# Performance work log

Hardware: AMD Instinct MI355X
Metric: run time of the kernel (lower is better)

Reference implementation:

```python
import jax, jax.numpy as jnp
import numpy as np

N = 50000
E = 800000
IN_C = 128
OUT_C = 256
NUM_REL = 6


def _rgcn_conv(x, src, dst, etype, W, root, bias):
    # PyG RGCNConv (no bases, aggr='mean'):
    # out = x @ root + bias + sum_r mean_{j in N_r(i)}(x_j) @ W[r]
    n = x.shape[0]
    xe = x[src]  # [E, d_in] gather of source features
    out = x @ root + bias
    for r in range(NUM_REL):
        m = (etype == r)
        s = jax.ops.segment_sum(jnp.where(m[:, None], xe, 0.0), dst, num_segments=n)
        c = jax.ops.segment_sum(m.astype(x.dtype), dst, num_segments=n)
        out = out + (s / jnp.maximum(c, 1.0)[:, None]) @ W[r]
    return out


def setup_inputs() -> dict:
    key = jax.random.key(0)
    ks = jax.random.split(key, 16)
    half = OUT_C // 2

    def g(k, shape, fan_in):
        return jax.random.normal(k, shape, dtype=jnp.float32) / np.sqrt(fan_in)

    return {
        "x": jax.random.normal(ks[0], (N, IN_C), dtype=jnp.float32),
        "edge_index": jax.random.randint(ks[1], (2, E), 0, N, dtype=jnp.int32),
        "edge_type": jax.random.randint(ks[2], (E,), 0, NUM_REL, dtype=jnp.int32),
        # encoder MLP
        "enc_w0": g(ks[3], (IN_C, OUT_C), IN_C), "enc_b0": jnp.zeros((OUT_C,), jnp.float32),
        "enc_w1": g(ks[4], (OUT_C, OUT_C), OUT_C), "enc_b1": jnp.zeros((OUT_C,), jnp.float32),
        "enc_w2": g(ks[5], (OUT_C, half), OUT_C), "enc_b2": jnp.zeros((half,), jnp.float32),
        # conv1
        "W1": g(ks[6], (NUM_REL, IN_C, OUT_C), IN_C), "root1": g(ks[7], (IN_C, OUT_C), IN_C),
        "b1": jnp.zeros((OUT_C,), jnp.float32),
        # conv2
        "W2": g(ks[8], (NUM_REL, OUT_C, OUT_C), OUT_C), "root2": g(ks[9], (OUT_C, OUT_C), OUT_C),
        "b2": jnp.zeros((OUT_C,), jnp.float32),
        # conv_out
        "W3": g(ks[10], (NUM_REL, OUT_C, half), OUT_C), "root3": g(ks[11], (OUT_C, half), OUT_C),
        "b3": jnp.zeros((half,), jnp.float32),
    }


def reference(x, edge_index, edge_type,
              enc_w0, enc_b0, enc_w1, enc_b1, enc_w2, enc_b2,
              W1, root1, b1, W2, root2, b2, W3, root3, b3):
    src, dst = edge_index[0], edge_index[1]
    # dense encoder branch
    h = jax.nn.relu(x @ enc_w0 + enc_b0)
    h = jax.nn.relu(h @ enc_w1 + enc_b1)
    self_feat = h @ enc_w2 + enc_b2
    # RGCN branch
    g1 = jax.nn.relu(_rgcn_conv(x, src, dst, edge_type, W1, root1, b1))
    g2 = jax.nn.relu(_rgcn_conv(g1, src, dst, edge_type, W2, root2, b2))
    graph_feat = _rgcn_conv(g2, src, dst, edge_type, W3, root3, b3)
    return jnp.concatenate([self_feat, graph_feat], axis=-1)
```

## Files before the change

kernel.cpp:

```cpp
#include <hip/hip_runtime.h>

#define NN   50000
#define EE   800000
#define INC  128
#define OUTC 256
#define HALF 128
#define NREL 6
#define NCELL (NN * NREL)

typedef __attribute__((ext_vector_type(4))) short s16x4;
typedef __attribute__((ext_vector_type(8))) short bf16x8;
typedef __attribute__((ext_vector_type(4))) float f32x4;

__device__ __forceinline__ float b2f(short b) {
    unsigned u = ((unsigned)(unsigned short)b) << 16;
    return __uint_as_float(u);
}
__device__ __forceinline__ short f2b(float f) {
    unsigned u = __float_as_uint(f);
    unsigned r = (u + 0x7fffu + ((u >> 16) & 1u)) >> 16;
    return (short)r;
}

__device__ __forceinline__ void gload16(const void* g, void* l) {
    __builtin_amdgcn_global_load_lds(
        (const __attribute__((address_space(1))) void*)g,
        (__attribute__((address_space(3))) void*)l, 16, 0, 0);
}

__global__ __launch_bounds__(256) void count_k(const int* __restrict__ dst,
                                               const int* __restrict__ et,
                                               int* __restrict__ cnt) {
    int e = blockIdx.x * 256 + threadIdx.x;
    if (e < EE) atomicAdd(&cnt[dst[e] * NREL + et[e]], 1);
}

__global__ __launch_bounds__(256) void scanA_k(const int* __restrict__ cnt,
                                               int* __restrict__ off,
                                               int* __restrict__ bsum, int n) {
    __shared__ int sh[256];
    int t = threadIdx.x;
    int base = blockIdx.x * 512 + t * 2;
    int v0 = (base < n) ? cnt[base] : 0;
    int v1 = (base + 1 < n) ? cnt[base + 1] : 0;
    int s = v0 + v1;
    sh[t] = s; __syncthreads();
    for (int o = 1; o < 256; o <<= 1) {
        int u = (t >= o) ? sh[t - o] : 0;
        __syncthreads();
        sh[t] += u;
        __syncthreads();
    }
    int excl = sh[t] - s;
    if (base < n)     off[base]     = excl;
    if (base + 1 < n) off[base + 1] = excl + v0;
    if (t == 255) bsum[blockIdx.x] = sh[255];
}

__global__ __launch_bounds__(1024) void scanB_k(int* __restrict__ bsum, int nb) {
    __shared__ int sh[1024];
    int t = threadIdx.x;
    int s = (t < nb) ? bsum[t] : 0;
    sh[t] = s; __syncthreads();
    for (int o = 1; o < 1024; o <<= 1) {
        int u = (t >= o) ? sh[t - o] : 0;
        __syncthreads();
        sh[t] += u;
        __syncthreads();
    }
    if (t < nb) bsum[t] = sh[t] - s;
}

__global__ __launch_bounds__(256) void scanC_k(int* __restrict__ off,
                                               const int* __restrict__ bsum, int n) {
    int i = blockIdx.x * 256 + threadIdx.x;
    if (i < n) off[i] += bsum[i >> 9];
    if (i == 0) off[n] = EE;
}

__global__ __launch_bounds__(256) void copyint_k(const int* __restrict__ a,
                                                 int* __restrict__ b, int n) {
    int i = blockIdx.x * 256 + threadIdx.x;
    if (i < n) b[i] = a[i];
}

__global__ __launch_bounds__(256) void fill_k(const int* __restrict__ src,
                                              const int* __restrict__ dst,
                                              const int* __restrict__ et,
                                              int* __restrict__ cur,
                                              int* __restrict__ es) {
    int e = blockIdx.x * 256 + threadIdx.x;
    if (e < EE) {
        int key = dst[e] * NREL + et[e];
        int p = atomicAdd(&cur[key], 1);
        es[p] = src[e];
    }
}

__global__ __launch_bounds__(256) void cast_x_k(const float* __restrict__ x,
                                                short* __restrict__ xb, int n4) {
    int i = blockIdx.x * 256 + threadIdx.x;
    if (i < n4) {
        float4 v = ((const float4*)x)[i];
        s16x4 o;
        o[0] = f2b(v.x); o[1] = f2b(v.y); o[2] = f2b(v.z); o[3] = f2b(v.w);
        ((s16x4*)xb)[i] = o;
    }
}

__global__ __launch_bounds__(256) void wtcat_k(const float* __restrict__ root,
                                               const float* __restrict__ W,
                                               int K0, int Ktot, int Ncols,
                                               short* __restrict__ WT) {
    int i = blockIdx.x * 256 + threadIdx.x;
    if (i >= Ncols * Ktot) return;
    int n = i / Ktot, k = i - n * Ktot;
    float v = (k < K0) ? root[(size_t)k * Ncols + n]
                       : W[(size_t)(k - K0) * Ncols + n];
    WT[(size_t)n * Ktot + k] = f2b(v);
}

template<int D>
__global__ __launch_bounds__(256) void agg_k(const short* __restrict__ X, int ldx,
                                             const int* __restrict__ off,
                                             const int* __restrict__ es,
                                             short* __restrict__ AG, int lda,
                                             int node0, int ncells) {
    constexpr int LPC = D / 4;
    int sub  = threadIdx.x / LPC;
    int lane = threadIdx.x % LPC;
    int ci = blockIdx.x * (256 / LPC) + sub;
    if (ci >= ncells) return;
    int node = ci / NREL, rel = ci - node * NREL;
    int gcell = (node0 + node) * NREL + rel;
    int beg = off[gcell], end = off[gcell + 1];
    int c0 = lane * 4;
    float s0 = 0.f, s1 = 0.f, s2 = 0.f, s3 = 0.f;
    int j = beg;
    for (; j + 1 < end; j += 2) {
        s16x4 v = *(const s16x4*)(X + (size_t)es[j] * ldx + c0);
        s16x4 w = *(const s16x4*)(X + (size_t)es[j + 1] * ldx + c0);
        s0 += b2f(v[0]) + b2f(w[0]);
        s1 += b2f(v[1]) + b2f(w[1]);
        s2 += b2f(v[2]) + b2f(w[2]);
        s3 += b2f(v[3]) + b2f(w[3]);
    }
    if (j < end) {
        s16x4 v = *(const s16x4*)(X + (size_t)es[j] * ldx + c0);
        s0 += b2f(v[0]); s1 += b2f(v[1]); s2 += b2f(v[2]); s3 += b2f(v[3]);
    }
    float inv = (end > beg) ? 1.f / (float)(end - beg) : 0.f;
    s16x4 o;
    o[0] = f2b(s0 * inv); o[1] = f2b(s1 * inv);
    o[2] = f2b(s2 * inv); o[3] = f2b(s3 * inv);
    *(s16x4*)(AG + (size_t)node * lda + rel * D + c0) = o;
}

#define ACH(R, q) ((((R) << 2) | ((q) ^ ((R) & 3) ^ (((R) >> 2) & 1))) * 8)

__global__ __launch_bounds__(256) void gemm_bt_k(
    const short* __restrict__ A0, int ld0,
    const short* __restrict__ A1, int ld1, int Ksplit,
    const short* __restrict__ BT,
    int M, int K, int Ncols,
    const float* __restrict__ bias, int relu,
    short* __restrict__ Cb, int ldcb,
    float* __restrict__ Cf, int ldcf) {
    __shared__ __align__(16) short As[2][128 * 32];
    __shared__ __align__(16) short Bs[2][128 * 32];
    const int tid = threadIdx.x;
    const int wave = tid >> 6, lane = tid & 63;
    const int wm = (wave & 1) * 64, wn = (wave >> 1) * 64;
    const int l16 = lane & 15, quad = lane >> 4;
    const int bm = blockIdx.x * 128, bn = blockIdx.y * 128;

    const int s0 = tid, s1 = tid + 256;
    const int r0 = s0 >> 2, c0 = (s0 & 3) ^ (r0 & 3) ^ ((r0 >> 2) & 1);
    const int r1 = s1 >> 2, c1 = (s1 & 3) ^ (r1 & 3) ^ ((r1 >> 2) & 1);

    auto stage = [&](int buf, int k0) {
        const short* Ab; int lda; int kk;
        if (k0 < Ksplit) { Ab = A0; lda = ld0; kk = k0; }
        else             { Ab = A1; lda = ld1; kk = k0 - Ksplit; }
        gload16(Ab + (size_t)(bm + r0) * lda + kk + c0 * 8, &As[buf][(wave * 64) * 8]);
        gload16(Ab + (size_t)(bm + r1) * lda + kk + c1 * 8, &As[buf][(256 + wave * 64) * 8]);
        gload16(BT + (size_t)(bn + r0) * K + k0 + c0 * 8,   &Bs[buf][(wave * 64) * 8]);
        gload16(BT + (size_t)(bn + r1) * K + k0 + c1 * 8,   &Bs[buf][(256 + wave * 64) * 8]);
    };

    f32x4 acc[4][4];
    #pragma unroll
    for (int i = 0; i < 4; ++i)
        #pragma unroll
        for (int j = 0; j < 4; ++j)
            acc[i][j] = (f32x4)0.f;

    stage(0, 0);
    const int nk = K >> 5;
    for (int it = 0; it < nk; ++it) {
        const int cur = it & 1;
        if (it + 1 < nk) {
            stage(cur ^ 1, (it + 1) << 5);
            asm volatile("s_waitcnt vmcnt(4)" ::: "memory");
        } else {
            asm volatile("s_waitcnt vmcnt(0)" ::: "memory");
        }
        __builtin_amdgcn_sched_barrier(0);
        __builtin_amdgcn_s_barrier();
        __builtin_amdgcn_sched_barrier(0);
        bf16x8 af[4], bf[4];
        #pragma unroll
        for (int mt = 0; mt < 4; ++mt)
            af[mt] = *(const bf16x8*)&As[cur][ACH(wm + mt * 16 + l16, quad)];
        #pragma unroll
        for (int nt = 0; nt < 4; ++nt)
            bf[nt] = *(const bf16x8*)&Bs[cur][ACH(wn + nt * 16 + l16, quad)];
        #pragma unroll
        for (int mt = 0; mt < 4; ++mt)
            #pragma unroll
            for (int nt = 0; nt < 4; ++nt)
                acc[mt][nt] = __builtin_amdgcn_mfma_f32_16x16x32_bf16(
                    af[mt], bf[nt], acc[mt][nt], 0, 0, 0);
        __builtin_amdgcn_sched_barrier(0);
        __builtin_amdgcn_s_barrier();
    }

    float bv[4];
    #pragma unroll
    for (int nt = 0; nt < 4; ++nt) bv[nt] = bias[bn + wn + nt * 16 + l16];

    #pragma unroll
    for (int mt = 0; mt < 4; ++mt) {
        int rb = bm + wm + mt * 16 + quad * 4;
        #pragma unroll
        for (int nt = 0; nt < 4; ++nt) {
            int gc = bn + wn + nt * 16 + l16;
            #pragma unroll
            for (int r = 0; r < 4; ++r) {
                int grow = rb + r;
                if (grow < M) {
                    float v = acc[mt][nt][r] + bv[nt];
                    if (relu) v = fmaxf(v, 0.f);
                    if (Cb) Cb[(size_t)grow * ldcb + gc] = f2b(v);
                    else    Cf[(size_t)grow * ldcf + gc] = v;
                }
            }
        }
    }
}

extern "C" void kernel_launch(void* const* d_in, const int* in_sizes, int n_in,
                              void* d_out, int out_size, void* d_ws, size_t ws_size,
                              hipStream_t stream) {
    const float* x      = (const float*)d_in[0];
    const int*   ei     = (const int*)d_in[1];
    const int*   srcv   = ei;
    const int*   dstv   = ei + EE;
    const int*   et     = (const int*)d_in[2];
    const float* enc_w0 = (const float*)d_in[3];
    const float* enc_b0 = (const float*)d_in[4];
    const float* enc_w1 = (const float*)d_in[5];
    const float* enc_b1 = (const float*)d_in[6];
    const float* enc_w2 = (const float*)d_in[7];
    const float* enc_b2 = (const float*)d_in[8];
    const float* W1     = (const float*)d_in[9];
    const float* root1  = (const float*)d_in[10];
    const float* b1     = (const float*)d_in[11];
    const float* W2     = (const float*)d_in[12];
    const float* root2  = (const float*)d_in[13];
    const float* b2     = (const float*)d_in[14];
    const float* W3     = (const float*)d_in[15];
    const float* root3  = (const float*)d_in[16];
    const float* b3     = (const float*)d_in[17];
    float* out = (float*)d_out;

    const int NPAD = 50048;

    char* p = (char*)d_ws;
    auto alloc = [&](size_t bytes) -> char* {
        char* r = p; p += (bytes + 255) & ~(size_t)255; return r;
    };
    short* xb  = (short*)alloc((size_t)NPAD * INC * 2);
    short* g1  = (short*)alloc((size_t)NPAD * OUTC * 2);
    short* g2  = (short*)alloc((size_t)NPAD * OUTC * 2);
    short* WT1 = (short*)alloc((size_t)OUTC * 896 * 2);
    short* WT2 = (short*)alloc((size_t)OUTC * 1792 * 2);
    short* WT3 = (short*)alloc((size_t)HALF * 1792 * 2);
    short* ET0 = (short*)alloc((size_t)OUTC * INC * 2);
    short* ET1 = (short*)alloc((size_t)OUTC * OUTC * 2);
    short* ET2 = (short*)alloc((size_t)HALF * OUTC * 2);
    int* CNT  = (int*)alloc((size_t)NCELL * 4);
    int* OFF  = (int*)alloc((size_t)(NCELL + 1) * 4);
    int* CUR  = (int*)alloc((size_t)NCELL * 4);
    int* ES   = (int*)alloc((size_t)EE * 4);
    int* BSUM = (int*)alloc(1024 * 4);
    size_t fixed = (size_t)(p - (char*)d_ws);

    int chunk = 50000;
    if (fixed + (size_t)50048 * 1536 * 2 > ws_size) chunk = 25000;
    if (chunk == 25000 && fixed + (size_t)25088 * 1536 * 2 > ws_size) chunk = 12500;
    int crpad = ((chunk + 127) / 128) * 128;
    short* AG = (short*)alloc((size_t)crpad * 1536 * 2);

    hipMemsetAsync(CNT, 0, (size_t)NCELL * 4, stream);
    count_k<<<EE / 256, 256, 0, stream>>>(dstv, et, CNT);
    int nbA = (NCELL + 511) / 512;
    scanA_k<<<nbA, 256, 0, stream>>>(CNT, OFF, BSUM, NCELL);
    scanB_k<<<1, 1024, 0, stream>>>(BSUM, nbA);
    scanC_k<<<(NCELL + 255) / 256, 256, 0, stream>>>(OFF, BSUM, NCELL);
    copyint_k<<<(NCELL + 255) / 256, 256, 0, stream>>>(OFF, CUR, NCELL);
    fill_k<<<EE / 256, 256, 0, stream>>>(srcv, dstv, et, CUR, ES);

    cast_x_k<<<(NN * INC / 4 + 255) / 256, 256, 0, stream>>>(x, xb, NN * INC / 4);
    wtcat_k<<<(OUTC * 896 + 255) / 256, 256, 0, stream>>>(root1, W1, INC, 896, OUTC, WT1);
    wtcat_k<<<(OUTC * 1792 + 255) / 256, 256, 0, stream>>>(root2, W2, OUTC, 1792, OUTC, WT2);
    wtcat_k<<<(HALF * 1792 + 255) / 256, 256, 0, stream>>>(root3, W3, OUTC, 1792, HALF, WT3);
    wtcat_k<<<(OUTC * INC + 255) / 256, 256, 0, stream>>>(enc_w0, nullptr, INC, INC, OUTC, ET0);
    wtcat_k<<<(OUTC * OUTC + 255) / 256, 256, 0, stream>>>(enc_w1, nullptr, OUTC, OUTC, OUTC, ET1);
    wtcat_k<<<(HALF * OUTC + 255) / 256, 256, 0, stream>>>(enc_w2, nullptr, OUTC, OUTC, HALF, ET2);

    auto gemm = [&](const short* A0, int ld0, const short* A1, int ld1, int Ksplit,
                    const short* BT, int M, int K, int Ncols,
                    const float* bias, int relu, short* Cb, int ldcb, float* Cf, int ldcf) {
        dim3 grid((M + 127) / 128, Ncols / 128);
        gemm_bt_k<<<grid, 256, 0, stream>>>(A0, ld0, A1, ld1, Ksplit, BT,
                                            M, K, Ncols, bias, relu, Cb, ldcb, Cf, ldcf);
    };

    gemm(xb, INC, nullptr, 0, INC, ET0, NN, INC, OUTC, enc_b0, 1, g1, OUTC, nullptr, 0);
    gemm(g1, OUTC, nullptr, 0, OUTC, ET1, NN, OUTC, OUTC, enc_b1, 1, g2, OUTC, nullptr, 0);
    gemm(g2, OUTC, nullptr, 0, OUTC, ET2, NN, OUTC, HALF, enc_b2, 0, nullptr, 0, out, OUTC);

    for (int c0 = 0; c0 < NN; c0 += chunk) {
        int nc = chunk * NREL;
        agg_k<INC><<<(nc + 7) / 8, 256, 0, stream>>>(xb, INC, OFF, ES, AG, 768, c0, nc);
        gemm(xb + (size_t)c0 * INC, INC, AG, 768, INC, WT1, chunk, 896, OUTC,
             b1, 1, g1 + (size_t)c0 * OUTC, OUTC, nullptr, 0);
    }
    for (int c0 = 0; c0 < NN; c0 += chunk) {
        int nc = chunk * NREL;
        agg_k<OUTC><<<(nc + 3) / 4, 256, 0, stream>>>(g1, OUTC, OFF, ES, AG, 1536, c0, nc);
        gemm(g1 + (size_t)c0 * OUTC, OUTC, AG, 1536, OUTC, WT2, chunk, 1792, OUTC,
             b2, 1, g2 + (size_t)c0 * OUTC, OUTC, nullptr, 0);
    }
    for (int c0 = 0; c0 < NN; c0 += chunk) {
        int nc = chunk * NREL;
        agg_k<OUTC><<<(nc + 3) / 4, 256, 0, stream>>>(g2, OUTC, OFF, ES, AG, 1536, c0, nc);
        gemm(g2 + (size_t)c0 * OUTC, OUTC, AG, 1536, OUTC, WT3, chunk, 1792, HALF,
             b3, 0, nullptr, 0, out + (size_t)c0 * OUTC + HALF, OUTC);
    }
}
```

Baseline: 773.7 us.

## Triple-buffer GEMM pipeline and add 128x64 tile variant for narrow outputs

Switches the bf16 MFMA GEMM from double to triple buffering of shared-memory tiles, prefetching two k-steps ahead with adjusted vmcnt waits to hide global-load latency. It also templates the kernel on the N-tile width, launching a 128x64 tile for 128-column outputs so those GEMMs get twice as many blocks. In exchange, shared memory per block rises, which may lower occupancy, and the narrow tile reuses each A tile across fewer output columns.

```diff
diff --git a/kernel.cpp b/kernel.cpp
--- a/kernel.cpp
+++ b/kernel.cpp
@@ -157,7 +157,9 @@
 }
 
 #define ACH(R, q) ((((R) << 2) | ((q) ^ ((R) & 3) ^ (((R) >> 2) & 1))) * 8)
-
+#define WAITV(N) asm volatile("s_waitcnt vmcnt(" #N ")" ::: "memory")
+
+template<int BN>
 __global__ __launch_bounds__(256) void gemm_bt_k(
     const short* __restrict__ A0, int ld0,
     const short* __restrict__ A1, int ld1, int Ksplit,
@@ -166,13 +168,16 @@
     const float* __restrict__ bias, int relu,
     short* __restrict__ Cb, int ldcb,
     float* __restrict__ Cf, int ldcf) {
-    __shared__ __align__(16) short As[2][128 * 32];
-    __shared__ __align__(16) short Bs[2][128 * 32];
+    constexpr int NBUF = 3;
+    constexpr int MT = (BN == 128) ? 4 : 2;
+    __shared__ __align__(16) short As[NBUF * 128 * 32];
+    __shared__ __align__(16) short Bs[NBUF * BN * 32];
     const int tid = threadIdx.x;
     const int wave = tid >> 6, lane = tid & 63;
-    const int wm = (wave & 1) * 64, wn = (wave >> 1) * 64;
     const int l16 = lane & 15, quad = lane >> 4;
-    const int bm = blockIdx.x * 128, bn = blockIdx.y * 128;
+    const int bm = blockIdx.x * 128, bn = blockIdx.y * BN;
+    const int wm = (BN == 128) ? (wave & 1) * 64 : wave * 32;
+    const int wn = (BN == 128) ? (wave >> 1) * 64 : 0;
 
     const int s0 = tid, s1 = tid + 256;
     const int r0 = s0 >> 2, c0 = (s0 & 3) ^ (r0 & 3) ^ ((r0 >> 2) & 1);
@@ -182,41 +187,49 @@
         const short* Ab; int lda; int kk;
         if (k0 < Ksplit) { Ab = A0; lda = ld0; kk = k0; }
         else             { Ab = A1; lda = ld1; kk = k0 - Ksplit; }
-        gload16(Ab + (size_t)(bm + r0) * lda + kk + c0 * 8, &As[buf][(wave * 64) * 8]);
-        gload16(Ab + (size_t)(bm + r1) * lda + kk + c1 * 8, &As[buf][(256 + wave * 64) * 8]);
-        gload16(BT + (size_t)(bn + r0) * K + k0 + c0 * 8,   &Bs[buf][(wave * 64) * 8]);
-        gload16(BT + (size_t)(bn + r1) * K + k0 + c1 * 8,   &Bs[buf][(256 + wave * 64) * 8]);
+        short* at = As + buf * (128 * 32);
+        short* bt = Bs + buf * (BN * 32);
+        gload16(Ab + (size_t)(bm + r0) * lda + kk + c0 * 8, at + (wave * 64) * 8);
+        gload16(Ab + (size_t)(bm + r1) * lda + kk + c1 * 8, at + (256 + wave * 64) * 8);
+        gload16(BT + (size_t)(bn + r0) * K + k0 + c0 * 8, bt + (wave * 64) * 8);
+        if (BN == 128)
+            gload16(BT + (size_t)(bn + r1) * K + k0 + c1 * 8, bt + (256 + wave * 64) * 8);
     };
 
-    f32x4 acc[4][4];
+    f32x4 acc[MT][4];
     #pragma unroll
-    for (int i = 0; i < 4; ++i)
+    for (int i = 0; i < MT; ++i)
         #pragma unroll
         for (int j = 0; j < 4; ++j)
             acc[i][j] = (f32x4)0.f;
 
+    const int nk = K >> 5;
     stage(0, 0);
-    const int nk = K >> 5;
+    if (nk > 1) stage(1, 32);
     for (int it = 0; it < nk; ++it) {
-        const int cur = it & 1;
-        if (it + 1 < nk) {
-            stage(cur ^ 1, (it + 1) << 5);
-            asm volatile("s_waitcnt vmcnt(4)" ::: "memory");
+        const int cur = it % NBUF;
+        if (it + 2 < nk) {
+            stage((it + 2) % NBUF, (it + 2) << 5);
+            if (BN == 128) { WAITV(8); } else { WAITV(6); }
+        } else if (it + 1 < nk) {
+            if (BN == 128) { WAITV(4); } else { WAITV(3); }
         } else {
-            asm volatile("s_waitcnt vmcnt(0)" ::: "memory");
+            WAITV(0);
         }
         __builtin_amdgcn_sched_barrier(0);
         __builtin_amdgcn_s_barrier();
         __builtin_amdgcn_sched_barrier(0);
-        bf16x8 af[4], bf[4];
-        #pragma unroll
-        for (int mt = 0; mt < 4; ++mt)
-            af[mt] = *(const bf16x8*)&As[cur][ACH(wm + mt * 16 + l16, quad)];
+        const short* at = As + cur * (128 * 32);
+        const short* bt = Bs + cur * (BN * 32);
+        bf16x8 af[MT], bf[4];
+        #pragma unroll
+        for (int mt = 0; mt < MT; ++mt)
+            af[mt] = *(const bf16x8*)&at[ACH(wm + mt * 16 + l16, quad)];
         #pragma unroll
         for (int nt = 0; nt < 4; ++nt)
-            bf[nt] = *(const bf16x8*)&Bs[cur][ACH(wn + nt * 16 + l16, quad)];
-        #pragma unroll
-        for (int mt = 0; mt < 4; ++mt)
+            bf[nt] = *(const bf16x8*)&bt[ACH(wn + nt * 16 + l16, quad)];
+        #pragma unroll
+        for (int mt = 0; mt < MT; ++mt)
             #pragma unroll
             for (int nt = 0; nt < 4; ++nt)
                 acc[mt][nt] = __builtin_amdgcn_mfma_f32_16x16x32_bf16(
@@ -230,7 +243,7 @@
     for (int nt = 0; nt < 4; ++nt) bv[nt] = bias[bn + wn + nt * 16 + l16];
 
     #pragma unroll
-    for (int mt = 0; mt < 4; ++mt) {
+    for (int mt = 0; mt < MT; ++mt) {
         int rb = bm + wm + mt * 16 + quad * 4;
         #pragma unroll
         for (int nt = 0; nt < 4; ++nt) {
@@ -322,9 +335,15 @@
     auto gemm = [&](const short* A0, int ld0, const short* A1, int ld1, int Ksplit,
                     const short* BT, int M, int K, int Ncols,
                     const float* bias, int relu, short* Cb, int ldcb, float* Cf, int ldcf) {
-        dim3 grid((M + 127) / 128, Ncols / 128);
-        gemm_bt_k<<<grid, 256, 0, stream>>>(A0, ld0, A1, ld1, Ksplit, BT,
-                                            M, K, Ncols, bias, relu, Cb, ldcb, Cf, ldcf);
+        if (Ncols >= 256) {
+            dim3 grid((M + 127) / 128, Ncols / 128);
+            gemm_bt_k<128><<<grid, 256, 0, stream>>>(A0, ld0, A1, ld1, Ksplit, BT,
+                                                     M, K, Ncols, bias, relu, Cb, ldcb, Cf, ldcf);
+        } else {
+            dim3 grid((M + 127) / 128, Ncols / 64);
+            gemm_bt_k<64><<<grid, 256, 0, stream>>>(A0, ld0, A1, ld1, Ksplit, BT,
+                                                    M, K, Ncols, bias, relu, Cb, ldcb, Cf, ldcf);
+        }
     };
 
     gemm(xb, INC, nullptr, 0, INC, ET0, NN, INC, OUTC, enc_b0, 1, g1, OUTC, nullptr, 0);
```

Measured after the change: 787.6 us. Within noise of the previous version (+1.8%).
